# Kernel optimization log

Measured on AMD Instinct MI355X. Metric: run time of the kernel, lower is better.

## Reference

```python
import jax, jax.numpy as jnp
import numpy as np


def setup_inputs() -> dict:
    key = jax.random.key(0)
    k1, k2, k3, k4 = jax.random.split(key, 4)
    d_in, d_out, r = 4096, 4096, 16
    n_tok = 8192  # batch 4 * seq 2048
    x = jax.random.normal(k1, (n_tok, d_in), dtype=jnp.float32)
    W = jax.random.normal(k2, (d_out, d_in), dtype=jnp.float32)
    A = jax.random.normal(k3, (d_out, r), dtype=jnp.float32)
    B = jax.random.normal(k4, (r, d_in), dtype=jnp.float32)
    return {"x": x, "W": W, "A": A, "B": B}


def reference(x, W, A, B):
    # Faithful to torch: F.linear(x, W + A @ B) = x @ (W + A @ B)^T, no bias.
    W_eff = W + A @ B  # [d_out, d_in], materialized as in the original module
    return x @ W_eff.T  # [n_tok, d_out]
```

## Files before the change

kernel.cpp:

```cpp
#include <hip/hip_runtime.h>

typedef __attribute__((ext_vector_type(8))) short short8;
typedef __attribute__((ext_vector_type(4))) float f32x4;
typedef unsigned short ushort_t;

#define BAR()   __builtin_amdgcn_s_barrier()
#define LGKM0() asm volatile("s_waitcnt lgkmcnt(0)" ::: "memory")
#define LGKM8() asm volatile("s_waitcnt lgkmcnt(8)" ::: "memory")
#define VM6()   asm volatile("s_waitcnt vmcnt(6)" ::: "memory")
#define VM0()   asm volatile("s_waitcnt vmcnt(0)" ::: "memory")
#define PRIO(n) __builtin_amdgcn_s_setprio(n)
#define MFMA(a_, b_, c_) __builtin_amdgcn_mfma_f32_16x16x32_bf16(a_, b_, c_, 0, 0, 0)

__device__ __forceinline__ unsigned short f2bf(float f) {
  unsigned u = __builtin_bit_cast(unsigned, f);
  u += 0x7FFFu + ((u >> 16) & 1u);
  return (unsigned short)(u >> 16);
}

__device__ __forceinline__ void gl_lds16(const void* g, void* l) {
  __builtin_amdgcn_global_load_lds(
      (const __attribute__((address_space(1))) void*)g,
      (__attribute__((address_space(3))) void*)l, 16, 0, 0);
}

__global__ __launch_bounds__(256) void cvt_x(const float* __restrict__ x,
                                             ushort_t* __restrict__ xb) {
  size_t i = ((size_t)blockIdx.x * 256 + threadIdx.x) * 8;
  float4 v0 = *(const float4*)(x + i);
  float4 v1 = *(const float4*)(x + i + 4);
  union { ushort_t s[8]; uint4 v; } o;
  o.s[0] = f2bf(v0.x); o.s[1] = f2bf(v0.y); o.s[2] = f2bf(v0.z); o.s[3] = f2bf(v0.w);
  o.s[4] = f2bf(v1.x); o.s[5] = f2bf(v1.y); o.s[6] = f2bf(v1.z); o.s[7] = f2bf(v1.w);
  *(uint4*)(xb + i) = o.v;
}

__global__ __launch_bounds__(256) void build_weff(const float* __restrict__ W,
                                                  const float* __restrict__ A,
                                                  const float* __restrict__ B,
                                                  ushort_t* __restrict__ Weff) {
  const int K = 4096, R = 16;
  const int n = blockIdx.y;
  const int k = (blockIdx.x * 256 + threadIdx.x) * 4;
  float4 w = *(const float4*)(W + (size_t)n * K + k);
  float a0 = w.x, a1 = w.y, a2 = w.z, a3 = w.w;
#pragma unroll
  for (int r = 0; r < R; ++r) {
    float a = A[n * R + r];
    float4 b = *(const float4*)(B + (size_t)r * K + k);
    a0 += a * b.x; a1 += a * b.y; a2 += a * b.z; a3 += a * b.w;
  }
  union { ushort_t s[4]; uint2 v; } o;
  o.s[0] = f2bf(a0); o.s[1] = f2bf(a1); o.s[2] = f2bf(a2); o.s[3] = f2bf(a3);
  *(uint2*)(Weff + (size_t)n * K + k) = o.v;
}


__device__ __forceinline__ void stage_half(const ushort_t* __restrict__ G, int grow0, int kc,
                                           ushort_t* half, int tid) {
#pragma unroll
  for (int r = 0; r < 2; ++r) {
    const int P = (r * 512 + tid) * 16;
    const int L = P ^ (((P >> 9) & 1) << 5);
    const int row = L >> 7;
    const int colb = L & 127;
    const ushort_t* src = G + (size_t)(grow0 + row) * 4096 + kc + (colb >> 1);
    char* dst = (char*)half + (size_t)((r * 512 + (tid & ~63)) * 16);
    gl_lds16(src, dst);
  }
}

__global__ __launch_bounds__(512) void gemm256(const ushort_t* __restrict__ Xb,
                                               const ushort_t* __restrict__ Wb,
                                               float* __restrict__ C) {
  const int N = 4096;
  const int NT = 4096 / 64;
  __shared__ __align__(16) ushort_t lds[2][4][128 * 64];

  const int tid = threadIdx.x;
  const int l   = tid & 63;
  const int w   = tid >> 6;
  const int wm  = w >> 2;
  const int wn  = w & 3;

  const int bid = blockIdx.x;
  const int c = bid & 7, q = bid >> 3;
  const int tm = (c >> 1) * 8 + (q >> 3);
  const int tn = (c & 1) * 8 + (q & 7);
  const int bm = tm * 256, bn = tn * 256;

  const int rb = (((l & 15) * 128) + ((l >> 4) * 16)) ^ (((l >> 2) & 1) << 5);

  f32x4 acc[8][4];
#pragma unroll
  for (int i = 0; i < 8; ++i)
#pragma unroll
    for (int j = 0; j < 4; ++j) acc[i][j] = (f32x4)(0.0f);

  stage_half(Wb, bn,       0,  lds[0][2], tid);
  stage_half(Xb, bm,       0,  lds[0][0], tid);
  stage_half(Wb, bn + 128, 0,  lds[0][3], tid);
  stage_half(Xb, bm + 128, 0,  lds[0][1], tid);
  stage_half(Wb, bn,       64, lds[1][2], tid);
  stage_half(Xb, bm,       64, lds[1][0], tid);
  stage_half(Wb, bn + 128, 64, lds[1][3], tid);
  VM6();
  BAR();

  short8 a[8][2];
  short8 bb[2][2];

#define RD(P_) (*(const short8*)(P_))

  int cur = 0;
  for (int t = 0; t < NT; ++t) {
    const char* Ab = (const char*)lds[cur][wm] + rb;
    const char* Bb = (const char*)lds[cur][2 + (wn >> 1)] + (wn & 1) * 8192 + rb;
    const int kc1 = (t + 1) * 64, kc2 = (t + 2) * 64;

#pragma unroll
    for (int mi = 0; mi < 4; ++mi) {
      a[mi][0] = RD(Ab + mi * 2048);
      a[mi][1] = RD(Ab + mi * 2048 + 64);
    }
#pragma unroll
    for (int ni = 0; ni < 2; ++ni) {
      bb[ni][0] = RD(Bb + ni * 2048);
      bb[ni][1] = RD(Bb + ni * 2048 + 64);
    }
    if (t + 1 < NT) stage_half(Xb, bm + 128, kc1, lds[cur ^ 1][1], tid);
    LGKM8();
    BAR(); LGKM0(); PRIO(1);
#pragma unroll
    for (int kh = 0; kh < 2; ++kh)
#pragma unroll
      for (int mi = 0; mi < 4; ++mi)
#pragma unroll
        for (int ni = 0; ni < 2; ++ni)
          acc[mi][ni] = MFMA(a[mi][kh], bb[ni][kh], acc[mi][ni]);
    PRIO(0); BAR();

#pragma unroll
    for (int mi = 4; mi < 8; ++mi) {
      a[mi][0] = RD(Ab + mi * 2048);
      a[mi][1] = RD(Ab + mi * 2048 + 64);
    }
    BAR(); LGKM0(); PRIO(1);
#pragma unroll
    for (int kh = 0; kh < 2; ++kh)
#pragma unroll
      for (int mi = 4; mi < 8; ++mi)
#pragma unroll
        for (int ni = 0; ni < 2; ++ni)
          acc[mi][ni] = MFMA(a[mi][kh], bb[ni][kh], acc[mi][ni]);
    PRIO(0); BAR();

#pragma unroll
    for (int ni = 0; ni < 2; ++ni) {
      bb[ni][0] = RD(Bb + (2 + ni) * 2048);
      bb[ni][1] = RD(Bb + (2 + ni) * 2048 + 64);
    }
    if (t + 2 < NT) stage_half(Xb, bm, kc2, lds[cur][0], tid);
    BAR(); LGKM0(); PRIO(1);
#pragma unroll
    for (int kh = 0; kh < 2; ++kh)
#pragma unroll
      for (int mi = 0; mi < 4; ++mi)
#pragma unroll
        for (int ni = 0; ni < 2; ++ni)
          acc[mi][ni + 2] = MFMA(a[mi][kh], bb[ni][kh], acc[mi][ni + 2]);
    PRIO(0); BAR();

    if (t + 2 < NT) {
      stage_half(Wb, bn,       kc2, lds[cur][2], tid);
      stage_half(Wb, bn + 128, kc2, lds[cur][3], tid);
      VM6();
    } else {
      VM0();
    }
    BAR(); PRIO(1);
#pragma unroll
    for (int kh = 0; kh < 2; ++kh)
#pragma unroll
      for (int mi = 4; mi < 8; ++mi)
#pragma unroll
        for (int ni = 0; ni < 2; ++ni)
          acc[mi][ni + 2] = MFMA(a[mi][kh], bb[ni][kh], acc[mi][ni + 2]);
    PRIO(0); BAR();

    cur ^= 1;
  }

  const int erow = bm + wm * 128 + (l >> 4) * 4;
  const int ecol = bn + wn * 64 + (l & 15);
#pragma unroll
  for (int mi = 0; mi < 8; ++mi) {
#pragma unroll
    for (int ni = 0; ni < 4; ++ni) {
      float* cp = C + (size_t)(erow + mi * 16) * N + ecol + ni * 16;
#pragma unroll
      for (int j = 0; j < 4; ++j) cp[(size_t)j * N] = acc[mi][ni][j];
    }
  }
}

extern "C" void kernel_launch(void* const* d_in, const int* in_sizes, int n_in,
                              void* d_out, int out_size, void* d_ws, size_t ws_size,
                              hipStream_t stream) {
  const float* x = (const float*)d_in[0];
  const float* W = (const float*)d_in[1];
  const float* A = (const float*)d_in[2];
  const float* B = (const float*)d_in[3];
  float* out = (float*)d_out;

  ushort_t* xb = (ushort_t*)d_ws;
  ushort_t* wb = (ushort_t*)((char*)d_ws + (size_t)8192 * 4096 * 2);

  cvt_x<<<16384, 256, 0, stream>>>(x, xb);
  dim3 gw(4, 4096);
  build_weff<<<gw, 256, 0, stream>>>(W, A, B, wb);
  gemm256<<<512, 512, 0, stream>>>(xb, wb, out);
}
```

Baseline: 344.8 us.

## Switch GEMM to 32x32x16 MFMA with K-split LDS tile layout

Replaces the 16x16x32 bf16 MFMA tiles with 32x32x16 MFMAs, so each wave holds four by two 32x32 accumulators instead of eight by four 16x16 ones. The LDS staging is reorganised so each buffer half holds 256 rows by 32 K-columns, with a new XOR swizzle and new read offsets. The intent is fewer LDS fragment reads per FLOP and higher MFMA throughput per instruction. The in-loop staging order and waitcnt placement change to match, and the epilogue is rewritten for the 32x32 output lane layout.

```diff
diff --git a/kernel.cpp b/kernel.cpp
--- a/kernel.cpp
+++ b/kernel.cpp
@@ -1,16 +1,15 @@
 #include <hip/hip_runtime.h>
 
 typedef __attribute__((ext_vector_type(8))) short short8;
-typedef __attribute__((ext_vector_type(4))) float f32x4;
+typedef __attribute__((ext_vector_type(16))) float f32x16;
 typedef unsigned short ushort_t;
 
 #define BAR()   __builtin_amdgcn_s_barrier()
 #define LGKM0() asm volatile("s_waitcnt lgkmcnt(0)" ::: "memory")
-#define LGKM8() asm volatile("s_waitcnt lgkmcnt(8)" ::: "memory")
 #define VM6()   asm volatile("s_waitcnt vmcnt(6)" ::: "memory")
 #define VM0()   asm volatile("s_waitcnt vmcnt(0)" ::: "memory")
 #define PRIO(n) __builtin_amdgcn_s_setprio(n)
-#define MFMA(a_, b_, c_) __builtin_amdgcn_mfma_f32_16x16x32_bf16(a_, b_, c_, 0, 0, 0)
+#define MFMA32(a_, b_, c_) __builtin_amdgcn_mfma_f32_32x32x16_bf16(a_, b_, c_, 0, 0, 0)
 
 __device__ __forceinline__ unsigned short f2bf(float f) {
   unsigned u = __builtin_bit_cast(unsigned, f);
@@ -56,16 +55,15 @@
 }
 
 
-__device__ __forceinline__ void stage_half(const ushort_t* __restrict__ G, int grow0, int kc,
+__device__ __forceinline__ void stage_half(const ushort_t* __restrict__ G, int row0, int kc,
                                            ushort_t* half, int tid) {
 #pragma unroll
   for (int r = 0; r < 2; ++r) {
-    const int P = (r * 512 + tid) * 16;
-    const int L = P ^ (((P >> 9) & 1) << 5);
-    const int row = L >> 7;
-    const int colb = L & 127;
-    const ushort_t* src = G + (size_t)(grow0 + row) * 4096 + kc + (colb >> 1);
-    char* dst = (char*)half + (size_t)((r * 512 + (tid & ~63)) * 16);
+    const int idx  = r * 512 + tid;
+    const int lrow = idx >> 2;
+    const int cb   = ((idx & 3) * 16) ^ (((lrow >> 3) & 1) << 5);
+    const ushort_t* src = G + (size_t)(row0 + lrow) * 4096 + kc + (cb >> 1);
+    char* dst = (char*)half + (size_t)(r * 512 + (tid & ~63)) * 16;
     gl_lds16(src, dst);
   }
 }
@@ -75,7 +73,7 @@
                                                float* __restrict__ C) {
   const int N = 4096;
   const int NT = 4096 / 64;
-  __shared__ __align__(16) ushort_t lds[2][4][128 * 64];
+  __shared__ __align__(16) ushort_t lds[2][4][256 * 32];
 
   const int tid = threadIdx.x;
   const int l   = tid & 63;
@@ -89,117 +87,127 @@
   const int tn = (c & 1) * 8 + (q & 7);
   const int bm = tm * 256, bn = tn * 256;
 
-  const int rb = (((l & 15) * 128) + ((l >> 4) * 16)) ^ (((l >> 2) & 1) << 5);
-
-  f32x4 acc[8][4];
-#pragma unroll
-  for (int i = 0; i < 8; ++i)
-#pragma unroll
-    for (int j = 0; j < 4; ++j) acc[i][j] = (f32x4)(0.0f);
-
-  stage_half(Wb, bn,       0,  lds[0][2], tid);
-  stage_half(Xb, bm,       0,  lds[0][0], tid);
-  stage_half(Wb, bn + 128, 0,  lds[0][3], tid);
-  stage_half(Xb, bm + 128, 0,  lds[0][1], tid);
-  stage_half(Wb, bn,       64, lds[1][2], tid);
-  stage_half(Xb, bm,       64, lds[1][0], tid);
-  stage_half(Wb, bn + 128, 64, lds[1][3], tid);
+  const int colb0 = ((l >> 5) * 16) ^ (((l >> 3) & 1) << 5);
+  int aoff[4], boff[2];
+#pragma unroll
+  for (int mi = 0; mi < 4; ++mi) aoff[mi] = (wm * 128 + mi * 32 + (l & 31)) * 64 + colb0;
+#pragma unroll
+  for (int ni = 0; ni < 2; ++ni) boff[ni] = (wn * 64 + ni * 32 + (l & 31)) * 64 + colb0;
+
+  f32x16 acc[4][2];
+#pragma unroll
+  for (int i = 0; i < 4; ++i)
+#pragma unroll
+    for (int j = 0; j < 2; ++j) acc[i][j] = (f32x16)(0.0f);
+
+  stage_half(Wb, bn, 0,  lds[0][2], tid);
+  stage_half(Xb, bm, 0,  lds[0][0], tid);
+  stage_half(Wb, bn, 32, lds[0][3], tid);
+  stage_half(Xb, bm, 32, lds[0][1], tid);
+  stage_half(Wb, bn, 64, lds[1][2], tid);
+  stage_half(Xb, bm, 64, lds[1][0], tid);
+  stage_half(Wb, bn, 96, lds[1][3], tid);
   VM6();
   BAR();
 
-  short8 a[8][2];
-  short8 bb[2][2];
+  short8 a01[2][2], a23[2][2], bb[2][2];
 
 #define RD(P_) (*(const short8*)(P_))
 
   int cur = 0;
   for (int t = 0; t < NT; ++t) {
-    const char* Ab = (const char*)lds[cur][wm] + rb;
-    const char* Bb = (const char*)lds[cur][2 + (wn >> 1)] + (wn & 1) * 8192 + rb;
-    const int kc1 = (t + 1) * 64, kc2 = (t + 2) * 64;
-
-#pragma unroll
-    for (int mi = 0; mi < 4; ++mi) {
-      a[mi][0] = RD(Ab + mi * 2048);
-      a[mi][1] = RD(Ab + mi * 2048 + 64);
-    }
-#pragma unroll
-    for (int ni = 0; ni < 2; ++ni) {
-      bb[ni][0] = RD(Bb + ni * 2048);
-      bb[ni][1] = RD(Bb + ni * 2048 + 64);
-    }
-    if (t + 1 < NT) stage_half(Xb, bm + 128, kc1, lds[cur ^ 1][1], tid);
-    LGKM8();
-    BAR(); LGKM0(); PRIO(1);
-#pragma unroll
-    for (int kh = 0; kh < 2; ++kh)
-#pragma unroll
-      for (int mi = 0; mi < 4; ++mi)
-#pragma unroll
-        for (int ni = 0; ni < 2; ++ni)
-          acc[mi][ni] = MFMA(a[mi][kh], bb[ni][kh], acc[mi][ni]);
-    PRIO(0); BAR();
-
-#pragma unroll
-    for (int mi = 4; mi < 8; ++mi) {
-      a[mi][0] = RD(Ab + mi * 2048);
-      a[mi][1] = RD(Ab + mi * 2048 + 64);
-    }
-    BAR(); LGKM0(); PRIO(1);
-#pragma unroll
-    for (int kh = 0; kh < 2; ++kh)
-#pragma unroll
-      for (int mi = 4; mi < 8; ++mi)
-#pragma unroll
-        for (int ni = 0; ni < 2; ++ni)
-          acc[mi][ni] = MFMA(a[mi][kh], bb[ni][kh], acc[mi][ni]);
-    PRIO(0); BAR();
-
-#pragma unroll
-    for (int ni = 0; ni < 2; ++ni) {
-      bb[ni][0] = RD(Bb + (2 + ni) * 2048);
-      bb[ni][1] = RD(Bb + (2 + ni) * 2048 + 64);
-    }
+    const char* A0h = (const char*)lds[cur][0];
+    const char* A1h = (const char*)lds[cur][1];
+    const char* B0h = (const char*)lds[cur][2];
+    const char* B1h = (const char*)lds[cur][3];
+    const int kc2 = (t + 2) * 64;
+
+#pragma unroll
+    for (int mi = 0; mi < 2; ++mi)
+#pragma unroll
+      for (int ks = 0; ks < 2; ++ks) a01[mi][ks] = RD(A0h + (aoff[mi] ^ (ks << 5)));
+#pragma unroll
+    for (int ni = 0; ni < 2; ++ni)
+#pragma unroll
+      for (int ks = 0; ks < 2; ++ks) bb[ni][ks] = RD(B0h + (boff[ni] ^ (ks << 5)));
+    if (t + 1 < NT) stage_half(Xb, bm, (t + 1) * 64 + 32, lds[cur ^ 1][1], tid);
+    BAR(); LGKM0(); PRIO(1);
+#pragma unroll
+    for (int ks = 0; ks < 2; ++ks)
+#pragma unroll
+      for (int mi = 0; mi < 2; ++mi)
+#pragma unroll
+        for (int ni = 0; ni < 2; ++ni)
+          acc[mi][ni] = MFMA32(a01[mi][ks], bb[ni][ks], acc[mi][ni]);
+    PRIO(0); BAR();
+
+#pragma unroll
+    for (int mi = 0; mi < 2; ++mi)
+#pragma unroll
+      for (int ks = 0; ks < 2; ++ks) a23[mi][ks] = RD(A0h + (aoff[2 + mi] ^ (ks << 5)));
+    if (t + 2 < NT) stage_half(Wb, bn, kc2, lds[cur][2], tid);
+    BAR(); LGKM0(); PRIO(1);
+#pragma unroll
+    for (int ks = 0; ks < 2; ++ks)
+#pragma unroll
+      for (int mi = 0; mi < 2; ++mi)
+#pragma unroll
+        for (int ni = 0; ni < 2; ++ni)
+          acc[2 + mi][ni] = MFMA32(a23[mi][ks], bb[ni][ks], acc[2 + mi][ni]);
+    PRIO(0); BAR();
+
+#pragma unroll
+    for (int mi = 0; mi < 2; ++mi)
+#pragma unroll
+      for (int ks = 0; ks < 2; ++ks) a01[mi][ks] = RD(A1h + (aoff[mi] ^ (ks << 5)));
+#pragma unroll
+    for (int ni = 0; ni < 2; ++ni)
+#pragma unroll
+      for (int ks = 0; ks < 2; ++ks) bb[ni][ks] = RD(B1h + (boff[ni] ^ (ks << 5)));
     if (t + 2 < NT) stage_half(Xb, bm, kc2, lds[cur][0], tid);
     BAR(); LGKM0(); PRIO(1);
 #pragma unroll
-    for (int kh = 0; kh < 2; ++kh)
-#pragma unroll
-      for (int mi = 0; mi < 4; ++mi)
-#pragma unroll
-        for (int ni = 0; ni < 2; ++ni)
-          acc[mi][ni + 2] = MFMA(a[mi][kh], bb[ni][kh], acc[mi][ni + 2]);
-    PRIO(0); BAR();
-
+    for (int ks = 0; ks < 2; ++ks)
+#pragma unroll
+      for (int mi = 0; mi < 2; ++mi)
+#pragma unroll
+        for (int ni = 0; ni < 2; ++ni)
+          acc[mi][ni] = MFMA32(a01[mi][ks], bb[ni][ks], acc[mi][ni]);
+    PRIO(0); BAR();
+
+#pragma unroll
+    for (int mi = 0; mi < 2; ++mi)
+#pragma unroll
+      for (int ks = 0; ks < 2; ++ks) a23[mi][ks] = RD(A1h + (aoff[2 + mi] ^ (ks << 5)));
     if (t + 2 < NT) {
-      stage_half(Wb, bn,       kc2, lds[cur][2], tid);
-      stage_half(Wb, bn + 128, kc2, lds[cur][3], tid);
+      stage_half(Wb, bn, kc2 + 32, lds[cur][3], tid);
       VM6();
     } else {
       VM0();
     }
-    BAR(); PRIO(1);
-#pragma unroll
-    for (int kh = 0; kh < 2; ++kh)
-#pragma unroll
-      for (int mi = 4; mi < 8; ++mi)
-#pragma unroll
-        for (int ni = 0; ni < 2; ++ni)
-          acc[mi][ni + 2] = MFMA(a[mi][kh], bb[ni][kh], acc[mi][ni + 2]);
+    BAR(); LGKM0(); PRIO(1);
+#pragma unroll
+    for (int ks = 0; ks < 2; ++ks)
+#pragma unroll
+      for (int mi = 0; mi < 2; ++mi)
+#pragma unroll
+        for (int ni = 0; ni < 2; ++ni)
+          acc[2 + mi][ni] = MFMA32(a23[mi][ks], bb[ni][ks], acc[2 + mi][ni]);
     PRIO(0); BAR();
 
     cur ^= 1;
   }
 
-  const int erow = bm + wm * 128 + (l >> 4) * 4;
-  const int ecol = bn + wn * 64 + (l & 15);
-#pragma unroll
-  for (int mi = 0; mi < 8; ++mi) {
-#pragma unroll
-    for (int ni = 0; ni < 4; ++ni) {
-      float* cp = C + (size_t)(erow + mi * 16) * N + ecol + ni * 16;
-#pragma unroll
-      for (int j = 0; j < 4; ++j) cp[(size_t)j * N] = acc[mi][ni][j];
+  const int erow0 = bm + wm * 128 + 4 * (l >> 5);
+  const int ecol  = bn + wn * 64 + (l & 31);
+#pragma unroll
+  for (int mi = 0; mi < 4; ++mi) {
+#pragma unroll
+    for (int ni = 0; ni < 2; ++ni) {
+      float* cp = C + (size_t)(erow0 + mi * 32) * N + ecol + ni * 32;
+#pragma unroll
+      for (int r = 0; r < 16; ++r)
+        cp[(size_t)((r & 3) + 8 * (r >> 2)) * N] = acc[mi][ni][r];
     }
   }
 }
```

Measured after the change: 364.3 us. +5.7%, slower.
